# Kernel tuning notes

Measured on AMD Instinct MI355X. Metric: run time of the kernel, lower is better.

The kernel has to match this reference:

```python
import jax, jax.numpy as jnp
import numpy as np

B, C, H, W = 4, 16, 256, 256
O = 32
KH = KW = 3
PAD = 1


def setup_inputs() -> dict:
    key = jax.random.key(0)
    ks = jax.random.split(key, 6)
    d_in = C * KH * KW          # 144
    d_out = O * KH * KW         # 288
    s1 = 1.0 / np.sqrt(d_in)
    s2 = 1.0 / np.sqrt(O)
    return {
        "x": jax.random.normal(ks[0], (B, C, H, W), dtype=jnp.float32),
        "W1": jax.random.uniform(ks[1], (O, d_in), jnp.float32, -s1, s1),
        "b1": jax.random.uniform(ks[2], (O,), jnp.float32, -s1, s1),
        "W2": jax.random.uniform(ks[3], (d_out, O), jnp.float32, -s2, s2),
        "b2": jax.random.uniform(ks[4], (d_out,), jnp.float32, -s2, s2),
        "bias": jax.random.uniform(ks[5], (O,), jnp.float32, -s1, s1),
    }


def _unfold(x):
    """im2col matching torch F.unfold ordering (c, kh, kw): -> [B, H*W, C*KH*KW]."""
    b, c, h, w = x.shape
    xp = jnp.pad(x, ((0, 0), (0, 0), (PAD, PAD), (PAD, PAD)))
    # stack the KH*KW shifted views: [B, C, KH*KW, H, W]
    shifts = [xp[:, :, i:i + h, j:j + w] for i in range(KH) for j in range(KW)]
    p = jnp.stack(shifts, axis=2)
    # -> [B, H, W, C, KH*KW] -> [B, L, C*KH*KW]  (c-major, then (i,j))
    p = p.transpose(0, 3, 4, 1, 2)
    return p.reshape(b, h * w, c * KH * KW)


def reference(x, W1, b1, W2, b2, bias):
    b, c, h, w = x.shape
    L = h * w
    feat = _unfold(x)                                   # [B, L, C*9]
    # per-pixel kernel generator MLP
    hid = jnp.tanh(jnp.einsum('blf,of->blo', feat, W1) + b1)          # [B, L, O]
    kern = jnp.einsum('blo,go->blg', hid, W2) + b2                    # [B, L, O*9]
    kern = kern.reshape(b, L, O, KH * KW)                             # [B, L, O, 9]
    # contract per-pixel kernel with its patch (channels summed):
    # out[b,l,o] = sum_{c,i,j} K[b,l,o,ij] * P[b,l,c,ij]
    patch_c = feat.reshape(b, L, c, KH * KW).sum(axis=2)              # [B, L, 9]
    out = jnp.einsum('blok,blk->blo', kern, patch_c)                  # [B, L, O]
    out = out.transpose(0, 2, 1).reshape(b, O, h, w)
    return out + bias[None, :, None, None]
```

## Files before the change

kernel.cpp:

```cpp
#include <hip/hip_runtime.h>

#define CC 16
#define OO 32
#define LL 65536

typedef __attribute__((ext_vector_type(8))) short bf16x8;
typedef __attribute__((ext_vector_type(4))) float f32x4;
typedef __attribute__((ext_vector_type(4))) int   i32x4;

static __device__ __forceinline__ ushort f2b(float f) {
    union { float f; unsigned u; } v; v.f = f;
    return (ushort)((v.u + 0x7fff + ((v.u >> 16) & 1)) >> 16);
}
static __device__ __forceinline__ unsigned pk2(float fl, float fh) {
    unsigned ul = __float_as_uint(fl) + 0x8000u;
    unsigned uh = __float_as_uint(fh) + 0x8000u;
    return __builtin_amdgcn_perm(uh, ul, 0x07060302);
}

__global__ void prepass(const float* __restrict__ W1, const float* __restrict__ b1,
                        const float* __restrict__ W2, const float* __restrict__ b2,
                        const float* __restrict__ bias,
                        ushort* __restrict__ w1f, ushort* __restrict__ w2f) {
    int idx = blockIdx.x * 256 + threadIdx.x;
    if (idx < 5120) {
        int f = idx >> 9, lane = (idx >> 3) & 63, j = idx & 7;
        int ks = f >> 1, ot = f & 1, lm = lane & 15, g = lane >> 4;
        int o = ot * 16 + lm, kk = ks * 32 + g * 8 + j;
        int r = kk >> 4, c = kk & 15;
        float v = (kk < 144) ? W1[o * 144 + c * 9 + r] : (kk == 144 ? b1[o] : 0.f);
        w1f[idx] = f2b(v);
    } else if (idx < 15360) {
        int i2 = idx - 5120;
        int f = i2 >> 9, lane = (i2 >> 3) & 63, j = i2 & 7;
        int ks = f >> 1, ot = f & 1, lm = lane & 15, g = lane >> 4;
        int o = ot * 16 + lm, kk = ks * 32 + g * 8 + j;
        float v;
        if      (kk < 288) v = W2[o * 288 + kk];
        else if (kk < 297) v = b2[o * 9 + (kk - 288)];
        else if (kk == 297) v = bias[o];
        else               v = 0.f;
        w2f[i2] = f2b(v);
    }
}

__global__ __launch_bounds__(256, 2) void dynaconv_mfma(
    const float* __restrict__ x, const ushort* __restrict__ w1f,
    const ushort* __restrict__ w2f, float* __restrict__ out)
{
    __shared__ __align__(16) ushort xs[3][260][24];
    __shared__ __align__(16) float  S[3][260];
    __shared__ __align__(16) float  hidT[4][16][36];

    const int tid  = threadIdx.x;
    const int wv   = tid >> 6;
    const int lane = tid & 63;
    const int g    = lane >> 4;
    const int lm   = lane & 15;
    const int b    = blockIdx.x >> 8;
    const int h    = blockIdx.x & 255;

    bf16x8 W1R[10], W2R[20];
#pragma unroll
    for (int f = 0; f < 10; ++f) W1R[f] = *(const bf16x8*)(w1f + (f * 64 + lane) * 8);
#pragma unroll
    for (int f = 0; f < 20; ++f) W2R[f] = *(const bf16x8*)(w2f + (f * 64 + lane) * 8);

    const float* xb = x + b * (CC * LL);
    {
        float s0 = 0.f, s1 = 0.f, s2 = 0.f;
#pragma unroll
        for (int cp = 0; cp < 8; ++cp) {
            const float* p0 = xb + (2 * cp) * LL;
            const float* p1 = p0 + LL;
#pragma unroll
            for (int r = 0; r < 3; ++r) {
                const int hh = h - 1 + r;
                const bool ok = (unsigned)hh < 256u;
                const int off = (ok ? hh : 0) * 256 + tid;
                float va = p0[off], vb = p1[off];
                va = ok ? va : 0.f; vb = ok ? vb : 0.f;
                if (r == 0) s0 += va + vb; else if (r == 1) s1 += va + vb; else s2 += va + vb;
                *(unsigned*)&xs[r][tid + 1][2 * cp] = pk2(va, vb);
            }
        }
        S[0][tid + 1] = s0; S[1][tid + 1] = s1; S[2][tid + 1] = s2;
        if (tid < 96) {
            int r = tid >> 5, side = (tid >> 4) & 1, c = tid & 15;
            xs[r][side * 257][c] = 0;
        }
        if (tid < 6) S[tid >> 1][(tid & 1) * 257] = 0.f;
    }
    __syncthreads();

    int soff[5];
#pragma unroll
    for (int ks = 0; ks < 5; ++ks) {
        int r = 2 * ks + (g >> 1); if (r > 8) r = 8;
        int r3 = (r * 11) >> 5, rm = r - 3 * r3;
        soff[ks] = (r3 * 260 + rm + lm) * 24 + (g & 1) * 8;
    }
    const ushort* xsf = &xs[0][0][0];

#pragma unroll
    for (int t = 0; t < 4; ++t) {
        const int w0t = wv * 64 + t * 16;
        const int tb = w0t * 24;

        f32x4 a1[2] = {{0.f,0.f,0.f,0.f},{0.f,0.f,0.f,0.f}};
#pragma unroll
        for (int ks = 0; ks < 5; ++ks) {
            bf16x8 ff = *(const bf16x8*)(xsf + soff[ks] + tb);
            if (ks == 4) {
                i32x4 wd = *(i32x4*)&ff;
                wd[0] = (g < 2) ? wd[0] : (g == 2 ? 0x3F80 : 0);
                wd[1] = (g < 2) ? wd[1] : 0;
                wd[2] = (g < 2) ? wd[2] : 0;
                wd[3] = (g < 2) ? wd[3] : 0;
                ff = *(bf16x8*)&wd;
            }
            a1[0] = __builtin_amdgcn_mfma_f32_16x16x32_bf16(W1R[2 * ks],     ff, a1[0], 0, 0, 0);
            a1[1] = __builtin_amdgcn_mfma_f32_16x16x32_bf16(W1R[2 * ks + 1], ff, a1[1], 0, 0, 0);
        }

#pragma unroll
        for (int ot = 0; ot < 2; ++ot)
#pragma unroll
            for (int q = 0; q < 4; ++q) {
                float e = __expf(2.f * a1[ot][q]);
                hidT[wv][lm][ot * 16 + g * 4 + q] = 1.f - 2.f / (e + 1.f);
            }
        f32x4 h0 = *(const f32x4*)&hidT[wv][lm][g * 8];
        f32x4 h1 = *(const f32x4*)&hidT[wv][lm][g * 8 + 4];

        float pcv[9];
#pragma unroll
        for (int r = 0; r < 9; ++r) pcv[r] = S[r / 3][w0t + lm + (r % 3)];

        f32x4 a2[2] = {{0.f,0.f,0.f,0.f},{0.f,0.f,0.f,0.f}};
#pragma unroll
        for (int ks = 0; ks < 9; ++ks) {
            const float p = pcv[ks];
            i32x4 wd;
            wd[0] = (int)pk2(h0[0] * p, h0[1] * p);
            wd[1] = (int)pk2(h0[2] * p, h0[3] * p);
            wd[2] = (int)pk2(h1[0] * p, h1[1] * p);
            wd[3] = (int)pk2(h1[2] * p, h1[3] * p);
            bf16x8 ff2 = *(bf16x8*)&wd;
            a2[0] = __builtin_amdgcn_mfma_f32_16x16x32_bf16(W2R[2 * ks],     ff2, a2[0], 0, 0, 0);
            a2[1] = __builtin_amdgcn_mfma_f32_16x16x32_bf16(W2R[2 * ks + 1], ff2, a2[1], 0, 0, 0);
        }
        {
            i32x4 wd;
            wd[0] = (g == 0) ? (int)pk2(pcv[0], pcv[1]) : ((g == 1) ? (int)pk2(pcv[8], 1.f) : 0);
            wd[1] = (g == 0) ? (int)pk2(pcv[2], pcv[3]) : 0;
            wd[2] = (g == 0) ? (int)pk2(pcv[4], pcv[5]) : 0;
            wd[3] = (g == 0) ? (int)pk2(pcv[6], pcv[7]) : 0;
            bf16x8 ff2 = *(bf16x8*)&wd;
            a2[0] = __builtin_amdgcn_mfma_f32_16x16x32_bf16(W2R[18], ff2, a2[0], 0, 0, 0);
            a2[1] = __builtin_amdgcn_mfma_f32_16x16x32_bf16(W2R[19], ff2, a2[1], 0, 0, 0);
        }

        float* ob = out + b * (OO * LL) + h * 256 + w0t + lm;
#pragma unroll
        for (int ot = 0; ot < 2; ++ot)
#pragma unroll
            for (int q = 0; q < 4; ++q)
                ob[(ot * 16 + g * 4 + q) * LL] = a2[ot][q];
    }
}

extern "C" void kernel_launch(void* const* d_in, const int* in_sizes, int n_in,
                              void* d_out, int out_size, void* d_ws, size_t ws_size,
                              hipStream_t stream) {
    const float* x    = (const float*)d_in[0];
    const float* W1   = (const float*)d_in[1];
    const float* b1   = (const float*)d_in[2];
    const float* W2   = (const float*)d_in[3];
    const float* b2   = (const float*)d_in[4];
    const float* bias = (const float*)d_in[5];
    float* out = (float*)d_out;

    ushort* w1f = (ushort*)d_ws;
    ushort* w2f = w1f + 5120;

    prepass<<<60, 256, 0, stream>>>(W1, b1, W2, b2, bias, w1f, w2f);
    dynaconv_mfma<<<1024, 256, 0, stream>>>(x, w1f, w2f, out);
}
```

Before: 32.45 us.

## Process two output rows per block with shared halo and XCD-aware block swizzle

Each block now computes two adjacent output rows, staging four input rows instead of three so the halo rows are shared. This cuts redundant global loads of x and halves how often each block loads its weight fragments into registers. Block IDs are remapped so consecutive virtual rows land on the same XCD for L2 locality, and output stores become nontemporal. The grid halves to 512 blocks, which lowers parallelism on a GPU with many CUs and adds a bit more LDS per block.

```diff
diff --git a/kernel.cpp b/kernel.cpp
--- a/kernel.cpp
+++ b/kernel.cpp
@@ -48,8 +48,8 @@
     const float* __restrict__ x, const ushort* __restrict__ w1f,
     const ushort* __restrict__ w2f, float* __restrict__ out)
 {
-    __shared__ __align__(16) ushort xs[3][260][24];
-    __shared__ __align__(16) float  S[3][260];
+    __shared__ __align__(16) ushort xs[4][260][24];
+    __shared__ __align__(16) float  S[4][260];
     __shared__ __align__(16) float  hidT[4][16][36];
 
     const int tid  = threadIdx.x;
@@ -57,8 +57,10 @@
     const int lane = tid & 63;
     const int g    = lane >> 4;
     const int lm   = lane & 15;
-    const int b    = blockIdx.x >> 8;
-    const int h    = blockIdx.x & 255;
+
+    const int vbid = (blockIdx.x & 7) * 64 + (blockIdx.x >> 3);
+    const int b    = vbid >> 7;
+    const int h0   = (vbid & 127) * 2;
 
     bf16x8 W1R[10], W2R[20];
 #pragma unroll
@@ -68,28 +70,30 @@
 
     const float* xb = x + b * (CC * LL);
     {
-        float s0 = 0.f, s1 = 0.f, s2 = 0.f;
+        int offr[4]; bool okr[4];
+#pragma unroll
+        for (int r = 0; r < 4; ++r) {
+            const int hh = h0 - 1 + r;
+            okr[r] = (unsigned)hh < 256u;
+            offr[r] = (okr[r] ? hh : 0) * 256 + tid;
+        }
+        float sr[4] = {0.f, 0.f, 0.f, 0.f};
 #pragma unroll
         for (int cp = 0; cp < 8; ++cp) {
             const float* p0 = xb + (2 * cp) * LL;
             const float* p1 = p0 + LL;
 #pragma unroll
-            for (int r = 0; r < 3; ++r) {
-                const int hh = h - 1 + r;
-                const bool ok = (unsigned)hh < 256u;
-                const int off = (ok ? hh : 0) * 256 + tid;
-                float va = p0[off], vb = p1[off];
-                va = ok ? va : 0.f; vb = ok ? vb : 0.f;
-                if (r == 0) s0 += va + vb; else if (r == 1) s1 += va + vb; else s2 += va + vb;
+            for (int r = 0; r < 4; ++r) {
+                float va = p0[offr[r]], vb = p1[offr[r]];
+                va = okr[r] ? va : 0.f; vb = okr[r] ? vb : 0.f;
+                sr[r] += va + vb;
                 *(unsigned*)&xs[r][tid + 1][2 * cp] = pk2(va, vb);
             }
         }
-        S[0][tid + 1] = s0; S[1][tid + 1] = s1; S[2][tid + 1] = s2;
-        if (tid < 96) {
-            int r = tid >> 5, side = (tid >> 4) & 1, c = tid & 15;
-            xs[r][side * 257][c] = 0;
-        }
-        if (tid < 6) S[tid >> 1][(tid & 1) * 257] = 0.f;
+#pragma unroll
+        for (int r = 0; r < 4; ++r) S[r][tid + 1] = sr[r];
+        if (tid < 128) { int r = tid >> 5, side = (tid >> 4) & 1, c = tid & 15; xs[r][side * 257][c] = 0; }
+        if (tid < 8)   S[tid >> 1][(tid & 1) * 257] = 0.f;
     }
     __syncthreads();
 
@@ -102,71 +106,74 @@
     }
     const ushort* xsf = &xs[0][0][0];
 
+    for (int hr = 0; hr < 2; ++hr) {
+        const int hb = hr * (260 * 24);
 #pragma unroll
-    for (int t = 0; t < 4; ++t) {
-        const int w0t = wv * 64 + t * 16;
-        const int tb = w0t * 24;
+        for (int t = 0; t < 4; ++t) {
+            const int w0t = wv * 64 + t * 16;
+            const int tb = w0t * 24 + hb;
 
-        f32x4 a1[2] = {{0.f,0.f,0.f,0.f},{0.f,0.f,0.f,0.f}};
+            f32x4 a1[2] = {{0.f,0.f,0.f,0.f},{0.f,0.f,0.f,0.f}};
 #pragma unroll
-        for (int ks = 0; ks < 5; ++ks) {
-            bf16x8 ff = *(const bf16x8*)(xsf + soff[ks] + tb);
-            if (ks == 4) {
-                i32x4 wd = *(i32x4*)&ff;
-                wd[0] = (g < 2) ? wd[0] : (g == 2 ? 0x3F80 : 0);
-                wd[1] = (g < 2) ? wd[1] : 0;
-                wd[2] = (g < 2) ? wd[2] : 0;
-                wd[3] = (g < 2) ? wd[3] : 0;
-                ff = *(bf16x8*)&wd;
+            for (int ks = 0; ks < 5; ++ks) {
+                bf16x8 ff = *(const bf16x8*)(xsf + soff[ks] + tb);
+                if (ks == 4) {
+                    i32x4 wd = *(i32x4*)&ff;
+                    wd[0] = (g < 2) ? wd[0] : (g == 2 ? 0x3F80 : 0);
+                    wd[1] = (g < 2) ? wd[1] : 0;
+                    wd[2] = (g < 2) ? wd[2] : 0;
+                    wd[3] = (g < 2) ? wd[3] : 0;
+                    ff = *(bf16x8*)&wd;
+                }
+                a1[0] = __builtin_amdgcn_mfma_f32_16x16x32_bf16(W1R[2 * ks],     ff, a1[0], 0, 0, 0);
+                a1[1] = __builtin_amdgcn_mfma_f32_16x16x32_bf16(W1R[2 * ks + 1], ff, a1[1], 0, 0, 0);
             }
-            a1[0] = __builtin_amdgcn_mfma_f32_16x16x32_bf16(W1R[2 * ks],     ff, a1[0], 0, 0, 0);
-            a1[1] = __builtin_amdgcn_mfma_f32_16x16x32_bf16(W1R[2 * ks + 1], ff, a1[1], 0, 0, 0);
-        }
 
 #pragma unroll
-        for (int ot = 0; ot < 2; ++ot)
+            for (int ot = 0; ot < 2; ++ot)
 #pragma unroll
-            for (int q = 0; q < 4; ++q) {
-                float e = __expf(2.f * a1[ot][q]);
-                hidT[wv][lm][ot * 16 + g * 4 + q] = 1.f - 2.f / (e + 1.f);
+                for (int q = 0; q < 4; ++q) {
+                    float e = __expf(2.f * a1[ot][q]);
+                    hidT[wv][lm][ot * 16 + g * 4 + q] = 1.f - 2.f / (e + 1.f);
+                }
+            f32x4 h0v = *(const f32x4*)&hidT[wv][lm][g * 8];
+            f32x4 h1v = *(const f32x4*)&hidT[wv][lm][g * 8 + 4];
+
+            float pcv[9];
+#pragma unroll
+            for (int r = 0; r < 9; ++r) pcv[r] = S[r / 3 + hr][w0t + lm + (r % 3)];
+
+            f32x4 a2[2] = {{0.f,0.f,0.f,0.f},{0.f,0.f,0.f,0.f}};
+#pragma unroll
+            for (int ks = 0; ks < 9; ++ks) {
+                const float p = pcv[ks];
+                i32x4 wd;
+                wd[0] = (int)pk2(h0v[0] * p, h0v[1] * p);
+                wd[1] = (int)pk2(h0v[2] * p, h0v[3] * p);
+                wd[2] = (int)pk2(h1v[0] * p, h1v[1] * p);
+                wd[3] = (int)pk2(h1v[2] * p, h1v[3] * p);
+                bf16x8 ff2 = *(bf16x8*)&wd;
+                a2[0] = __builtin_amdgcn_mfma_f32_16x16x32_bf16(W2R[2 * ks],     ff2, a2[0], 0, 0, 0);
+                a2[1] = __builtin_amdgcn_mfma_f32_16x16x32_bf16(W2R[2 * ks + 1], ff2, a2[1], 0, 0, 0);
             }
-        f32x4 h0 = *(const f32x4*)&hidT[wv][lm][g * 8];
-        f32x4 h1 = *(const f32x4*)&hidT[wv][lm][g * 8 + 4];
+            {
+                i32x4 wd;
+                wd[0] = (g == 0) ? (int)pk2(pcv[0], pcv[1]) : ((g == 1) ? (int)pk2(pcv[8], 1.f) : 0);
+                wd[1] = (g == 0) ? (int)pk2(pcv[2], pcv[3]) : 0;
+                wd[2] = (g == 0) ? (int)pk2(pcv[4], pcv[5]) : 0;
+                wd[3] = (g == 0) ? (int)pk2(pcv[6], pcv[7]) : 0;
+                bf16x8 ff2 = *(bf16x8*)&wd;
+                a2[0] = __builtin_amdgcn_mfma_f32_16x16x32_bf16(W2R[18], ff2, a2[0], 0, 0, 0);
+                a2[1] = __builtin_amdgcn_mfma_f32_16x16x32_bf16(W2R[19], ff2, a2[1], 0, 0, 0);
+            }
 
-        float pcv[9];
+            float* ob = out + b * (OO * LL) + (h0 + hr) * 256 + w0t + lm;
 #pragma unroll
-        for (int r = 0; r < 9; ++r) pcv[r] = S[r / 3][w0t + lm + (r % 3)];
-
-        f32x4 a2[2] = {{0.f,0.f,0.f,0.f},{0.f,0.f,0.f,0.f}};
+            for (int ot = 0; ot < 2; ++ot)
 #pragma unroll
-        for (int ks = 0; ks < 9; ++ks) {
-            const float p = pcv[ks];
-            i32x4 wd;
-            wd[0] = (int)pk2(h0[0] * p, h0[1] * p);
-            wd[1] = (int)pk2(h0[2] * p, h0[3] * p);
-            wd[2] = (int)pk2(h1[0] * p, h1[1] * p);
-            wd[3] = (int)pk2(h1[2] * p, h1[3] * p);
-            bf16x8 ff2 = *(bf16x8*)&wd;
-            a2[0] = __builtin_amdgcn_mfma_f32_16x16x32_bf16(W2R[2 * ks],     ff2, a2[0], 0, 0, 0);
-            a2[1] = __builtin_amdgcn_mfma_f32_16x16x32_bf16(W2R[2 * ks + 1], ff2, a2[1], 0, 0, 0);
+                for (int q = 0; q < 4; ++q)
+                    __builtin_nontemporal_store(a2[ot][q], &ob[(ot * 16 + g * 4 + q) * LL]);
         }
-        {
-            i32x4 wd;
-            wd[0] = (g == 0) ? (int)pk2(pcv[0], pcv[1]) : ((g == 1) ? (int)pk2(pcv[8], 1.f) : 0);
-            wd[1] = (g == 0) ? (int)pk2(pcv[2], pcv[3]) : 0;
-            wd[2] = (g == 0) ? (int)pk2(pcv[4], pcv[5]) : 0;
-            wd[3] = (g == 0) ? (int)pk2(pcv[6], pcv[7]) : 0;
-            bf16x8 ff2 = *(bf16x8*)&wd;
-            a2[0] = __builtin_amdgcn_mfma_f32_16x16x32_bf16(W2R[18], ff2, a2[0], 0, 0, 0);
-            a2[1] = __builtin_amdgcn_mfma_f32_16x16x32_bf16(W2R[19], ff2, a2[1], 0, 0, 0);
-        }
-
-        float* ob = out + b * (OO * LL) + h * 256 + w0t + lm;
-#pragma unroll
-        for (int ot = 0; ot < 2; ++ot)
-#pragma unroll
-            for (int q = 0; q < 4; ++q)
-                ob[(ot * 16 + g * 4 + q) * LL] = a2[ot][q];
     }
 }
 
@@ -185,5 +192,5 @@
     ushort* w2f = w1f + 5120;
 
     prepass<<<60, 256, 0, stream>>>(W1, b1, W2, b2, bias, w1f, w2f);
-    dynaconv_mfma<<<1024, 256, 0, stream>>>(x, w1f, w2f, out);
+    dynaconv_mfma<<<512, 256, 0, stream>>>(x, w1f, w2f, out);
 }
```

Measured after the change: 26.83 us. 17.3% less time.

## Use 512-thread blocks, stage W2 in LDS, shuffle hidden activations, swizzle blocks

Applied to the files above, without the earlier changes.

Doubles the block to 512 threads so each wave handles two 16-column tiles instead of four. W2 fragments move from registers into shared memory, which frees VGPRs so the launch bound can ask for more blocks per CU. The hidden-layer transpose now uses bf16 packing and lane shuffles instead of an LDS round trip. The x row loads are split across thread halves, and the block index is remapped to change scheduling order. The cost is extra LDS traffic for the W2 reads on every MFMA and one extra bf16 rounding of the tanh output.

```diff
diff --git a/kernel.cpp b/kernel.cpp
--- a/kernel.cpp
+++ b/kernel.cpp
@@ -44,53 +44,76 @@
     }
 }
 
-__global__ __launch_bounds__(256, 2) void dynaconv_mfma(
+__global__ __launch_bounds__(512, 4) void dynaconv_mfma(
     const float* __restrict__ x, const ushort* __restrict__ w1f,
     const ushort* __restrict__ w2f, float* __restrict__ out)
 {
-    __shared__ __align__(16) ushort xs[3][260][24];
-    __shared__ __align__(16) float  S[3][260];
-    __shared__ __align__(16) float  hidT[4][16][36];
+    __shared__ __align__(16) ushort xs[3][258][24];
+    __shared__ __align__(16) float  S[3][258];
+    __shared__ __align__(16) ushort W2L[20 * 512];
 
     const int tid  = threadIdx.x;
     const int wv   = tid >> 6;
     const int lane = tid & 63;
     const int g    = lane >> 4;
     const int lm   = lane & 15;
-    const int b    = blockIdx.x >> 8;
-    const int h    = blockIdx.x & 255;
-
-    bf16x8 W1R[10], W2R[20];
+
+    const int vbid = (blockIdx.x & 7) * 128 + (blockIdx.x >> 3);
+    const int b    = vbid >> 8;
+    const int h    = vbid & 255;
+
+    bf16x8 W1R[10];
 #pragma unroll
     for (int f = 0; f < 10; ++f) W1R[f] = *(const bf16x8*)(w1f + (f * 64 + lane) * 8);
-#pragma unroll
-    for (int f = 0; f < 20; ++f) W2R[f] = *(const bf16x8*)(w2f + (f * 64 + lane) * 8);
+
+    {
+        const i32x4* src = (const i32x4*)w2f;
+        i32x4*       dst = (i32x4*)W2L;
+#pragma unroll
+        for (int k = 0; k < 3; ++k) {
+            int i = tid + k * 512;
+            if (i < 1280) dst[i] = src[i];
+        }
+    }
 
     const float* xb = x + b * (CC * LL);
-    {
-        float s0 = 0.f, s1 = 0.f, s2 = 0.f;
+    if (tid < 256) {
+        const int hm = h - 1;
+        const bool ok0 = hm >= 0;
+        const int off0 = (ok0 ? hm : 0) * 256 + tid;
+        const int off1 = h * 256 + tid;
+        float s0 = 0.f, s1 = 0.f;
 #pragma unroll
         for (int cp = 0; cp < 8; ++cp) {
             const float* p0 = xb + (2 * cp) * LL;
             const float* p1 = p0 + LL;
-#pragma unroll
-            for (int r = 0; r < 3; ++r) {
-                const int hh = h - 1 + r;
-                const bool ok = (unsigned)hh < 256u;
-                const int off = (ok ? hh : 0) * 256 + tid;
-                float va = p0[off], vb = p1[off];
-                va = ok ? va : 0.f; vb = ok ? vb : 0.f;
-                if (r == 0) s0 += va + vb; else if (r == 1) s1 += va + vb; else s2 += va + vb;
-                *(unsigned*)&xs[r][tid + 1][2 * cp] = pk2(va, vb);
-            }
-        }
-        S[0][tid + 1] = s0; S[1][tid + 1] = s1; S[2][tid + 1] = s2;
-        if (tid < 96) {
-            int r = tid >> 5, side = (tid >> 4) & 1, c = tid & 15;
-            xs[r][side * 257][c] = 0;
-        }
-        if (tid < 6) S[tid >> 1][(tid & 1) * 257] = 0.f;
-    }
+            float va0 = p0[off0], vb0 = p1[off0];
+            va0 = ok0 ? va0 : 0.f; vb0 = ok0 ? vb0 : 0.f;
+            float va1 = p0[off1], vb1 = p1[off1];
+            s0 += va0 + vb0; s1 += va1 + vb1;
+            *(unsigned*)&xs[0][tid + 1][2 * cp] = pk2(va0, vb0);
+            *(unsigned*)&xs[1][tid + 1][2 * cp] = pk2(va1, vb1);
+        }
+        S[0][tid + 1] = s0; S[1][tid + 1] = s1;
+    } else {
+        const int col = tid - 256;
+        const int hp = h + 1;
+        const bool ok2 = hp < 256;
+        const int off2 = (ok2 ? hp : 0) * 256 + col;
+        float s2 = 0.f;
+#pragma unroll
+        for (int cp = 0; cp < 8; ++cp) {
+            const float* p0 = xb + (2 * cp) * LL;
+            const float* p1 = p0 + LL;
+            float va = p0[off2], vb = p1[off2];
+            va = ok2 ? va : 0.f; vb = ok2 ? vb : 0.f;
+            s2 += va + vb;
+            *(unsigned*)&xs[2][col + 1][2 * cp] = pk2(va, vb);
+        }
+        S[2][col + 1] = s2;
+    }
+    if (tid < 96) { int r = tid >> 5, side = (tid >> 4) & 1, c = tid & 15; xs[r][side * 257][c] = 0; }
+    if (tid < 6)  S[tid >> 1][(tid & 1) * 257] = 0.f;
     __syncthreads();
 
     int soff[5];
@@ -98,13 +121,16 @@
     for (int ks = 0; ks < 5; ++ks) {
         int r = 2 * ks + (g >> 1); if (r > 8) r = 8;
         int r3 = (r * 11) >> 5, rm = r - 3 * r3;
-        soff[ks] = (r3 * 260 + rm + lm) * 24 + (g & 1) * 8;
+        soff[ks] = (r3 * 258 + rm + lm) * 24 + (g & 1) * 8;
     }
     const ushort* xsf = &xs[0][0][0];
-
-#pragma unroll
-    for (int t = 0; t < 4; ++t) {
-        const int w0t = wv * 64 + t * 16;
+    const int sA = ((g & 1) << 5) | lm;
+    const int sB = sA + 16;
+    const int hh = g >> 1;
+
+#pragma unroll
+    for (int t = 0; t < 2; ++t) {
+        const int w0t = wv * 32 + t * 16;
         const int tb = w0t * 24;
 
         f32x4 a1[2] = {{0.f,0.f,0.f,0.f},{0.f,0.f,0.f,0.f}};
@@ -123,15 +149,23 @@
             a1[1] = __builtin_amdgcn_mfma_f32_16x16x32_bf16(W1R[2 * ks + 1], ff, a1[1], 0, 0, 0);
         }
 
-#pragma unroll
-        for (int ot = 0; ot < 2; ++ot)
-#pragma unroll
-            for (int q = 0; q < 4; ++q) {
-                float e = __expf(2.f * a1[ot][q]);
-                hidT[wv][lm][ot * 16 + g * 4 + q] = 1.f - 2.f / (e + 1.f);
-            }
-        f32x4 h0 = *(const f32x4*)&hidT[wv][lm][g * 8];
-        f32x4 h1 = *(const f32x4*)&hidT[wv][lm][g * 8 + 4];
+        unsigned Wq[4];
+#pragma unroll
+        for (int q = 0; q < 4; ++q) {
+            float e0 = __expf(2.f * a1[0][q]);
+            float t0 = 1.f - 2.f / (e0 + 1.f);
+            float e1 = __expf(2.f * a1[1][q]);
+            float t1 = 1.f - 2.f / (e1 + 1.f);
+            Wq[q] = pk2(t0, t1);
+        }
+        float hf[8];
+#pragma unroll
+        for (int q = 0; q < 4; ++q) {
+            unsigned pa = (unsigned)__shfl((int)Wq[q], sA);
+            unsigned pb = (unsigned)__shfl((int)Wq[q], sB);
+            hf[q]     = __uint_as_float(hh ? (pa & 0xffff0000u) : (pa << 16));
+            hf[4 + q] = __uint_as_float(hh ? (pb & 0xffff0000u) : (pb << 16));
+        }
 
         float pcv[9];
 #pragma unroll
@@ -142,13 +176,15 @@
         for (int ks = 0; ks < 9; ++ks) {
             const float p = pcv[ks];
             i32x4 wd;
-            wd[0] = (int)pk2(h0[0] * p, h0[1] * p);
-            wd[1] = (int)pk2(h0[2] * p, h0[3] * p);
-            wd[2] = (int)pk2(h1[0] * p, h1[1] * p);
-            wd[3] = (int)pk2(h1[2] * p, h1[3] * p);
+            wd[0] = (int)pk2(hf[0] * p, hf[1] * p);
+            wd[1] = (int)pk2(hf[2] * p, hf[3] * p);
+            wd[2] = (int)pk2(hf[4] * p, hf[5] * p);
+            wd[3] = (int)pk2(hf[6] * p, hf[7] * p);
             bf16x8 ff2 = *(bf16x8*)&wd;
-            a2[0] = __builtin_amdgcn_mfma_f32_16x16x32_bf16(W2R[2 * ks],     ff2, a2[0], 0, 0, 0);
-            a2[1] = __builtin_amdgcn_mfma_f32_16x16x32_bf16(W2R[2 * ks + 1], ff2, a2[1], 0, 0, 0);
+            bf16x8 bm0 = *(const bf16x8*)(W2L + (2 * ks)     * 512 + lane * 8);
+            bf16x8 bm1 = *(const bf16x8*)(W2L + (2 * ks + 1) * 512 + lane * 8);
+            a2[0] = __builtin_amdgcn_mfma_f32_16x16x32_bf16(bm0, ff2, a2[0], 0, 0, 0);
+            a2[1] = __builtin_amdgcn_mfma_f32_16x16x32_bf16(bm1, ff2, a2[1], 0, 0, 0);
         }
         {
             i32x4 wd;
@@ -157,8 +193,10 @@
             wd[2] = (g == 0) ? (int)pk2(pcv[4], pcv[5]) : 0;
             wd[3] = (g == 0) ? (int)pk2(pcv[6], pcv[7]) : 0;
             bf16x8 ff2 = *(bf16x8*)&wd;
-            a2[0] = __builtin_amdgcn_mfma_f32_16x16x32_bf16(W2R[18], ff2, a2[0], 0, 0, 0);
-            a2[1] = __builtin_amdgcn_mfma_f32_16x16x32_bf16(W2R[19], ff2, a2[1], 0, 0, 0);
+            bf16x8 bm0 = *(const bf16x8*)(W2L + 18 * 512 + lane * 8);
+            bf16x8 bm1 = *(const bf16x8*)(W2L + 19 * 512 + lane * 8);
+            a2[0] = __builtin_amdgcn_mfma_f32_16x16x32_bf16(bm0, ff2, a2[0], 0, 0, 0);
+            a2[1] = __builtin_amdgcn_mfma_f32_16x16x32_bf16(bm1, ff2, a2[1], 0, 0, 0);
         }
 
         float* ob = out + b * (OO * LL) + h * 256 + w0t + lm;
@@ -185,5 +223,5 @@
     ushort* w2f = w1f + 5120;
 
     prepass<<<60, 256, 0, stream>>>(W1, b1, W2, b2, bias, w1f, w2f);
-    dynaconv_mfma<<<1024, 256, 0, stream>>>(x, w1f, w2f, out);
-}
+    dynaconv_mfma<<<1024, 512, 0, stream>>>(x, w1f, w2f, out);
+}
```

After: 29.91 us. -7.8%, faster.
